# Optimization experiments

Hardware: AMD Instinct MI355X
Metric: run time of the kernel (lower is better)

Reference implementation:

```python
import jax, jax.numpy as jnp
import numpy as np

G = 8  # order of C8 rotation group

def expand_circulant(w):
    # w: [out_fields, in_fields, G] free params of a C8 regular->regular 1x1 conv.
    # Full weight: W[of*G+go, if*G+gi] = w[of, if, (go-gi) mod G]
    g = jnp.arange(G)
    idx = (g[:, None] - g[None, :]) % G            # [go, gi]
    Wf = w[:, :, idx]                              # [of, if, go, gi]
    Wf = jnp.transpose(Wf, (0, 2, 1, 3))           # [of, go, if, gi]
    return Wf.reshape(w.shape[0] * G, w.shape[1] * G)

def eq_proj(x2, w, b):
    # x2: [B, in_fields*G]; equivariant 1x1 conv = GEMM with circulant-expanded weight
    Wf = expand_circulant(w)                       # [out_fields*G, in_fields*G]
    bf = jnp.repeat(b, G)                          # per-field bias, shared across group dim
    return x2 @ Wf.T + bf

def setup_inputs() -> dict:
    key = jax.random.key(0)
    ks = jax.random.split(key, 12)
    B, d_model, n_head, d_k, d_v = 8192, 128, 8, 64, 64
    C = d_model * G                                # 1024
    s_in = 0.02
    inp = {
        'q': jax.random.normal(ks[0], (B, C, 1, 1), jnp.float32),
        'k': jax.random.normal(ks[1], (B, C, 1, 1), jnp.float32),
        'v': jax.random.normal(ks[2], (B, C, 1, 1), jnp.float32),
        'w_q': jax.random.normal(ks[3], (n_head * d_k, d_model, G), jnp.float32) * s_in,
        'b_q': jnp.zeros((n_head * d_k,), jnp.float32),
        'w_k': jax.random.normal(ks[4], (n_head * d_k, d_model, G), jnp.float32) * s_in,
        'b_k': jnp.zeros((n_head * d_k,), jnp.float32),
        'w_v': jax.random.normal(ks[5], (n_head * d_v, d_model, G), jnp.float32) * s_in,
        'b_v': jnp.zeros((n_head * d_v,), jnp.float32),
        'w_fc': jax.random.normal(ks[6], (d_model, n_head * d_v, G), jnp.float32) * s_in,
        'b_fc': jnp.zeros((d_model,), jnp.float32),
    }
    return inp

def reference(q, k, v, w_q, b_q, w_k, b_k, w_v, b_v, w_fc, b_fc):
    B, C = q.shape[0], q.shape[1]
    n_head, d_k = 8, 64
    d_v = 64
    temp = jnp.asarray(d_k ** 0.5, q.dtype)
    residual = q                                   # [B, C, 1, 1]
    q2 = q.reshape(B, C)
    k2 = k.reshape(B, C)
    v2 = v.reshape(B, C)
    # equivariant 1x1 conv projections -> [B, n_head*d_k*G]
    qp = eq_proj(q2, w_q, b_q).reshape(B, G, n_head, d_k).transpose(0, 2, 1, 3)  # [B,H,G,dk]
    kp = eq_proj(k2, w_k, b_k).reshape(B, G, n_head, d_k).transpose(0, 2, 1, 3)
    vp = eq_proj(v2, w_v, b_v).reshape(B, G, n_head, d_v).transpose(0, 2, 1, 3)
    # scaled dot-product attention over the G=8 group/orientation positions
    attn = jax.nn.softmax(jnp.einsum('bhqd,bhkd->bhqk', qp / temp, kp), axis=-1)  # [B,H,G,G]
    out = jnp.einsum('bhqk,bhkd->bhqd', attn, vp)  # [B,H,G,dv]
    # transpose(1,2) then flatten, exactly as torch .view(sz_b, -1, 1, 1)
    out = out.transpose(0, 2, 1, 3).reshape(B, G * n_head * d_v)
    out = eq_proj(out, w_fc, b_fc)                 # [B, d_model*G]
    out = out.reshape(B, C, 1, 1) + residual
    return out, attn
```

## Files before the change

### kernel.cpp

```cpp
#include <hip/hip_runtime.h>
#include <hip/hip_bf16.h>

typedef unsigned short u16;
typedef unsigned int u32;
typedef __bf16 bf16x8_t __attribute__((ext_vector_type(8)));
typedef float f32x4_t __attribute__((ext_vector_type(4)));

#define BK 64

__device__ __forceinline__ float b2f(u16 v) {
  return __uint_as_float(((u32)v) << 16);
}
__device__ __forceinline__ u16 f2b(float f) {
  __hip_bfloat16 h = __float2bfloat16(f);
  return *reinterpret_cast<u16*>(&h);
}
__device__ __forceinline__ float blo(u32 u) { return __uint_as_float(u << 16); }
__device__ __forceinline__ float bhi(u32 u) { return __uint_as_float(u & 0xffff0000u); }

__device__ __forceinline__ void async_lds16(const u16* g, u16* l) {
  __builtin_amdgcn_global_load_lds(
      (__attribute__((address_space(1))) void*)g,
      (__attribute__((address_space(3))) void*)l, 16, 0, 0);
}

__device__ __forceinline__ void expand8(const float* __restrict__ w,
                                        u16* __restrict__ dst, int I,
                                        int kshift, int gid) {
  const int n = gid >> kshift;
  const int kc = (gid & ((1 << kshift) - 1)) * 8;
  const int K = 8 << kshift;
  const float* wp = w + (size_t)((n >> 3) * I + (kc >> 3)) * 8;
  float4 w0 = *(const float4*)wp;
  float4 w1 = *(const float4*)(wp + 4);
  float w8[8] = {w0.x, w0.y, w0.z, w0.w, w1.x, w1.y, w1.z, w1.w};
  u16 t[8];
  const int r = (n - kc) & 7;
#pragma unroll
  for (int j = 0; j < 8; ++j) t[j] = f2b(w8[(r - j) & 7]);
  *(uint4*)(dst + (size_t)n * K + kc) = *(const uint4*)t;
}

__device__ __forceinline__ void cvt8(const float* __restrict__ src,
                                     u16* __restrict__ dst, int gid) {
  const float* p = src + (size_t)gid * 8;
  float4 a = *(const float4*)p;
  float4 b = *(const float4*)(p + 4);
  u16 t[8] = {f2b(a.x), f2b(a.y), f2b(a.z), f2b(a.w),
              f2b(b.x), f2b(b.y), f2b(b.z), f2b(b.w)};
  *(uint4*)(dst + (size_t)gid * 8) = *(const uint4*)t;
}

__global__ __launch_bounds__(256) void expand_all(
    const float* __restrict__ w_q, const float* __restrict__ w_k,
    const float* __restrict__ w_v, const float* __restrict__ w_fc,
    const float* __restrict__ q, const float* __restrict__ k,
    const float* __restrict__ v, u16* __restrict__ Wq, u16* __restrict__ Wk,
    u16* __restrict__ Wv, u16* __restrict__ Wfc, u16* __restrict__ qb,
    u16* __restrict__ kb, u16* __restrict__ vb, int cblocks) {
  const int e = blockIdx.x;
  if (e < 8192) {
    const int plane = e >> 11;
    const int gid = (e & 2047) * 256 + threadIdx.x;
    if (plane == 0) expand8(w_q, Wq, 128, 7, gid);
    else if (plane == 1) expand8(w_k, Wk, 128, 7, gid);
    else if (plane == 2) expand8(w_v, Wv, 128, 7, gid);
    else expand8(w_fc, Wfc, 512, 9, gid);
  } else {
    const int ce = e - 8192;
    const int plane = ce / cblocks;
    const int gid = (ce - plane * cblocks) * 256 + threadIdx.x;
    if (plane == 0) cvt8(q, qb, gid);
    else if (plane == 1) cvt8(k, kb, gid);
    else cvt8(v, vb, gid);
  }
}

template <int TN, bool HAS_RES, bool OUT_F32>
__device__ __forceinline__ void gemm_core(
    const u16* __restrict__ Xb, const u16* __restrict__ W,
    const float* __restrict__ bias, const float* __restrict__ res,
    void* __restrict__ Yv, int M, int N, int K, int bid) {
  __shared__ __align__(16) u16 As[128 * BK];
  __shared__ __align__(16) u16 Bs[TN * BK];
  const int tid = threadIdx.x;

  const int grid_m = M >> 7, grid_n = N / TN;
  const int nb = grid_m * grid_n;
  int pid = (bid & 7) * (nb >> 3) + (bid >> 3);
  const int nig = 8 * grid_n;
  const int group_id = pid / nig;
  const int first_m = group_id * 8;
  const int gsz = min(8, grid_m - first_m);
  const int mt = first_m + (pid % gsz);
  const int nt = (pid % nig) / gsz;
  const int m0 = mt << 7, n0 = nt * TN;

  const int lane = tid & 63;
  const int wave = tid >> 6;
  const int wm = (wave >> 1) * 64;
  const int wn = (wave & 1) * (TN / 2);
  const int l16 = lane & 15;
  const int quad = lane >> 4;
  constexpr int NJ = TN >> 5;

  f32x4_t acc[4][NJ] = {};

  const int row0 = tid >> 3;
  const int kgl = ((tid & 7) ^ (row0 & 7)) * 8;

  for (int k0 = 0; k0 < K; k0 += BK) {
#pragma unroll
    for (int it = 0; it < TN / 32; ++it)
      async_lds16(W + (size_t)(n0 + row0 + it * 32) * K + (k0 + kgl),
                  &Bs[(tid + it * 256) * 8]);
#pragma unroll
    for (int it = 0; it < 4; ++it)
      async_lds16(Xb + (size_t)(m0 + row0 + it * 32) * K + (k0 + kgl),
                  &As[(tid + it * 256) * 8]);
    __syncthreads();
#pragma unroll
    for (int half = 0; half < 2; ++half) {
      bf16x8_t af[4], bfr[NJ];
#pragma unroll
      for (int i = 0; i < 4; ++i)
        af[i] = *(const bf16x8_t*)&As[(wm + i * 16 + l16) * BK +
                                      (((quad + half * 4) ^ (l16 & 7)) * 8)];
#pragma unroll
      for (int j = 0; j < NJ; ++j)
        bfr[j] = *(const bf16x8_t*)&Bs[(wn + j * 16 + l16) * BK +
                                       (((quad + half * 4) ^ (l16 & 7)) * 8)];
#pragma unroll
      for (int i = 0; i < 4; ++i)
#pragma unroll
        for (int j = 0; j < NJ; ++j)
          acc[i][j] =
              __builtin_amdgcn_mfma_f32_16x16x32_bf16(af[i], bfr[j], acc[i][j], 0, 0, 0);
    }
    __syncthreads();
  }

#pragma unroll
  for (int j = 0; j < NJ; ++j) {
    const int col = n0 + wn + j * 16 + l16;
    const float bv = bias[col >> 3];
#pragma unroll
    for (int i = 0; i < 4; ++i) {
#pragma unroll
      for (int r = 0; r < 4; ++r) {
        const int rw = m0 + wm + i * 16 + quad * 4 + r;
        float vv = acc[i][j][r] + bv;
        if (HAS_RES) vv += res[(size_t)rw * N + col];
        if (OUT_F32)
          ((float*)Yv)[(size_t)rw * N + col] = vv;
        else
          ((u16*)Yv)[(size_t)rw * N + col] = f2b(vv);
      }
    }
  }
}

__global__ __launch_bounds__(256) void gemm_qkv(
    const u16* __restrict__ X0, const u16* __restrict__ X1,
    const u16* __restrict__ X2, const u16* __restrict__ W0,
    const u16* __restrict__ W1, const u16* __restrict__ W2,
    const float* __restrict__ b0, const float* __restrict__ b1,
    const float* __restrict__ b2, u16* __restrict__ Y0, u16* __restrict__ Y1,
    u16* __restrict__ Y2, int M, int N, int K) {
  const int z = blockIdx.y;
  const u16* X = (z == 0) ? X0 : (z == 1) ? X1 : X2;
  const u16* W = (z == 0) ? W0 : (z == 1) ? W1 : W2;
  const float* bb = (z == 0) ? b0 : (z == 1) ? b1 : b2;
  u16* Y = (z == 0) ? Y0 : (z == 1) ? Y1 : Y2;
  gemm_core<128, false, false>(X, W, bb, nullptr, Y, M, N, K, blockIdx.x);
}

__global__ __launch_bounds__(256) void gemm_fc(
    const u16* __restrict__ X, const u16* __restrict__ W,
    const float* __restrict__ bias, const float* __restrict__ res,
    float* __restrict__ Y, int M, int N, int K) {
  gemm_core<128, true, true>(X, W, bias, res, Y, M, N, K, blockIdx.x);
}

__global__ __launch_bounds__(256) void attn_kernel(
    const u16* __restrict__ qp, const u16* __restrict__ kp,
    const u16* __restrict__ vp, float* __restrict__ probs,
    u16* __restrict__ o, int iters) {
  __shared__ __align__(16) u16 Qs[4][8 * 72];
  __shared__ __align__(16) u16 Ks[4][8 * 72];
  __shared__ __align__(16) float Ps[4][64];
  const int tid = threadIdx.x;
  const int wave = tid >> 6;
  const int lane = tid & 63;
  const int r = lane >> 3, c = lane & 7;
  const int ls = r * 72 + c * 8;
  const int qg = r;
  const int kg = c;

  auto pairof = [&](int it) { return (it * gridDim.x + blockIdx.x) * 4 + wave; };
  auto gaddr = [&](int it) {
    const int pr = pairof(it);
    return (size_t)(pr >> 3) * 4096 + (size_t)r * 512 + (pr & 7) * 64 + c * 8;
  };

  uint4 qr = *(const uint4*)(qp + gaddr(0));
  uint4 kr = *(const uint4*)(kp + gaddr(0));

  for (int it = 0; it < iters; ++it) {
    *(uint4*)&Qs[wave][ls] = qr;
    *(uint4*)&Ks[wave][ls] = kr;
    const int pair = pairof(it);
    const int b = pair >> 3;
    const int h = pair & 7;
    float vcf[8];
#pragma unroll
    for (int k2 = 0; k2 < 8; ++k2)
      vcf[k2] = b2f(vp[(size_t)b * 4096 + (size_t)k2 * 512 + h * 64 + lane]);
    if (it + 1 < iters) {
      qr = *(const uint4*)(qp + gaddr(it + 1));
      kr = *(const uint4*)(kp + gaddr(it + 1));
    }
    float s = 0.f;
#pragma unroll
    for (int d8 = 0; d8 < 8; ++d8) {
      uint4 qa = *(const uint4*)&Qs[wave][qg * 72 + d8 * 8];
      uint4 ka = *(const uint4*)&Ks[wave][kg * 72 + d8 * 8];
      s += blo(qa.x) * blo(ka.x) + bhi(qa.x) * bhi(ka.x);
      s += blo(qa.y) * blo(ka.y) + bhi(qa.y) * bhi(ka.y);
      s += blo(qa.z) * blo(ka.z) + bhi(qa.z) * bhi(ka.z);
      s += blo(qa.w) * blo(ka.w) + bhi(qa.w) * bhi(ka.w);
    }
    s *= 0.125f;
    float mx = s;
    mx = fmaxf(mx, __shfl_xor(mx, 1));
    mx = fmaxf(mx, __shfl_xor(mx, 2));
    mx = fmaxf(mx, __shfl_xor(mx, 4));
    float e = __expf(s - mx);
    float sum = e;
    sum += __shfl_xor(sum, 1);
    sum += __shfl_xor(sum, 2);
    sum += __shfl_xor(sum, 4);
    const float p = e / sum;
    probs[(size_t)pair * 64 + lane] = p;
    Ps[wave][lane] = p;
#pragma unroll
    for (int q2 = 0; q2 < 8; ++q2) {
      float4 p0 = *(const float4*)&Ps[wave][q2 * 8];
      float4 p1 = *(const float4*)&Ps[wave][q2 * 8 + 4];
      float acc = p0.x * vcf[0] + p0.y * vcf[1] + p0.z * vcf[2] + p0.w * vcf[3] +
                  p1.x * vcf[4] + p1.y * vcf[5] + p1.z * vcf[6] + p1.w * vcf[7];
      o[(size_t)b * 4096 + q2 * 512 + h * 64 + lane] = f2b(acc);
    }
  }
}

extern "C" void kernel_launch(void* const* d_in, const int* in_sizes, int n_in,
                              void* d_out, int out_size, void* d_ws, size_t ws_size,
                              hipStream_t stream) {
  const float* q = (const float*)d_in[0];
  const float* k = (const float*)d_in[1];
  const float* v = (const float*)d_in[2];
  const float* w_q = (const float*)d_in[3];
  const float* b_q = (const float*)d_in[4];
  const float* w_k = (const float*)d_in[5];
  const float* b_k = (const float*)d_in[6];
  const float* w_v = (const float*)d_in[7];
  const float* b_v = (const float*)d_in[8];
  const float* w_fc = (const float*)d_in[9];
  const float* b_fc = (const float*)d_in[10];

  const int B = in_sizes[0] / 1024;
  float* out = (float*)d_out;
  float* probs = out + (size_t)B * 1024;

  u16* Wq = (u16*)d_ws;
  u16* Wk = Wq + (size_t)4096 * 1024;
  u16* Wv = Wk + (size_t)4096 * 1024;
  u16* Wfc = Wv + (size_t)4096 * 1024;
  u16* qb = Wfc + (size_t)4096 * 1024;
  u16* kb = qb + (size_t)B * 1024;
  u16* vb = kb + (size_t)B * 1024;
  u16* scratch = vb + (size_t)B * 1024;
  const size_t fixed_bytes =
      ((size_t)4 * 4096 * 1024 + (size_t)3 * B * 1024) * sizeof(u16);

  const size_t per_row = (size_t)(4 * 4096) * sizeof(u16);
  int chunkB = 128;
  for (int c = B; c >= 128; c >>= 1) {
    if (fixed_bytes + (size_t)c * per_row <= ws_size) { chunkB = c; break; }
  }

  u16* qp = scratch;
  u16* kp = qp + (size_t)chunkB * 4096;
  u16* vp = kp + (size_t)chunkB * 4096;
  u16* ao = vp + (size_t)chunkB * 4096;

  const int cblocks = B / 2;
  expand_all<<<8192 + 3 * cblocks, 256, 0, stream>>>(
      w_q, w_k, w_v, w_fc, q, k, v, Wq, Wk, Wv, Wfc, qb, kb, vb, cblocks);

  for (int cs = 0; cs < B; cs += chunkB) {
    const int nb_p = (chunkB / 128) * (4096 / 128);
    gemm_qkv<<<dim3(nb_p, 3), 256, 0, stream>>>(
        qb + (size_t)cs * 1024, kb + (size_t)cs * 1024, vb + (size_t)cs * 1024,
        Wq, Wk, Wv, b_q, b_k, b_v, qp, kp, vp, chunkB, 4096, 1024);
    const int ablocks = (chunkB >= 1024) ? 2048 : chunkB * 2;
    const int aiters = (chunkB * 8) / (ablocks * 4);
    attn_kernel<<<ablocks, 256, 0, stream>>>(qp, kp, vp,
                                             probs + (size_t)cs * 512, ao, aiters);
    const int nb_fc = (chunkB / 128) * (1024 / 128);
    gemm_fc<<<nb_fc, 256, 0, stream>>>(ao, Wfc, b_fc, q + (size_t)cs * 1024,
                                       out + (size_t)cs * 1024, chunkB, 1024,
                                       4096);
  }
}
```

Baseline: 677.4 us.

## Add 256x256-tile 4-stage pipelined QKV GEMM and narrow FC GEMM tile

Replaces the QKV projection GEMM with a dedicated 512-thread kernel that uses 256x256 output tiles, BK=32, and a 4-deep asynchronous global-to-LDS pipeline with explicit vmcnt waits and MFMA priority boosting. Each wave now computes 128x64, which raises arithmetic intensity and hides memory latency behind more stages. The FC GEMM switches to 64-wide N tiles so it launches more blocks, and the minimum chunk size goes up to 256 to match the new tiling. The larger tile costs more registers and 128KB of LDS per block, which may limit occupancy.

```diff
diff --git a/kernel.cpp b/kernel.cpp
--- a/kernel.cpp
+++ b/kernel.cpp
@@ -76,6 +76,111 @@
   }
 }
 
+__global__ __launch_bounds__(512, 2) void gemm_qkv256(
+    const u16* __restrict__ X0, const u16* __restrict__ X1,
+    const u16* __restrict__ X2, const u16* __restrict__ W0,
+    const u16* __restrict__ W1, const u16* __restrict__ W2,
+    const float* __restrict__ b0, const float* __restrict__ b1,
+    const float* __restrict__ b2, u16* __restrict__ Y0, u16* __restrict__ Y1,
+    u16* __restrict__ Y2, int M, int N, int K) {
+  __shared__ __align__(16) u16 lds[4 * 16384];
+  const int z = blockIdx.y;
+  const u16* X = (z == 0) ? X0 : (z == 1) ? X1 : X2;
+  const u16* W = (z == 0) ? W0 : (z == 1) ? W1 : W2;
+  const float* bias = (z == 0) ? b0 : (z == 1) ? b1 : b2;
+  u16* Y = (z == 0) ? Y0 : (z == 1) ? Y1 : Y2;
+
+  const int tid = threadIdx.x;
+  const int bid = blockIdx.x;
+  const int grid_m = M >> 8, grid_n = N >> 8;
+  const int nb = grid_m * grid_n;
+  int pid = (bid & 7) * (nb >> 3) + (bid >> 3);
+  const int nig = 8 * grid_n;
+  const int group_id = pid / nig;
+  const int first_m = group_id * 8;
+  const int gsz = min(8, grid_m - first_m);
+  const int mt = first_m + (pid % gsz);
+  const int ntile = (pid % nig) / gsz;
+  const int m0 = mt << 8, n0 = ntile << 8;
+
+  const int lane = tid & 63, wave = tid >> 6;
+  const int wm = (wave >> 2) * 128;
+  const int wn = (wave & 3) * 64;
+  const int l16 = lane & 15, quad = lane >> 4;
+  const int kbl = quad ^ ((l16 >> 1) & 3);
+
+  const int srow = tid >> 2;
+  const int skbg = (tid & 3) ^ ((tid >> 3) & 3);
+  const u16* pA = X + (size_t)(m0 + srow) * K + skbg * 8;
+  const u16* pB = W + (size_t)(n0 + srow) * K + skbg * 8;
+  const size_t rskip = (size_t)128 * K;
+
+  const int aoff = (wm + l16) * 32 + kbl * 8;
+  const int boff = 8192 + (wn + l16) * 32 + kbl * 8;
+
+  f32x4_t acc[8][4] = {};
+  const int nt = K >> 5;
+
+  auto stage = [&](int t) {
+    u16* l = lds + (t & 3) * 16384;
+    const u16* a = pA + t * 32;
+    const u16* b = pB + t * 32;
+    async_lds16(a, l + tid * 8);
+    async_lds16(a + rskip, l + tid * 8 + 4096);
+    async_lds16(b, l + 8192 + tid * 8);
+    async_lds16(b + rskip, l + 8192 + tid * 8 + 4096);
+  };
+
+  stage(0);
+  __builtin_amdgcn_sched_barrier(0);
+  stage(1);
+  __builtin_amdgcn_sched_barrier(0);
+  stage(2);
+  asm volatile("s_waitcnt vmcnt(8)" ::: "memory");
+  __builtin_amdgcn_s_barrier();
+  __builtin_amdgcn_sched_barrier(0);
+
+  for (int t = 0; t < nt; ++t) {
+    if (t + 3 < nt) stage(t + 3);
+    const u16* la = lds + (t & 3) * 16384 + aoff;
+    const u16* lb = lds + (t & 3) * 16384 + boff;
+    bf16x8_t a[8], b[4];
+#pragma unroll
+    for (int mi = 0; mi < 8; ++mi) a[mi] = *(const bf16x8_t*)(la + mi * 512);
+#pragma unroll
+    for (int ni = 0; ni < 4; ++ni) b[ni] = *(const bf16x8_t*)(lb + ni * 512);
+    __builtin_amdgcn_s_setprio(1);
+#pragma unroll
+    for (int mi = 0; mi < 8; ++mi)
+#pragma unroll
+      for (int ni = 0; ni < 4; ++ni)
+        acc[mi][ni] = __builtin_amdgcn_mfma_f32_16x16x32_bf16(a[mi], b[ni],
+                                                              acc[mi][ni], 0, 0, 0);
+    __builtin_amdgcn_s_setprio(0);
+    if (t + 1 < nt) {
+      if (t + 3 < nt)      asm volatile("s_waitcnt vmcnt(8)" ::: "memory");
+      else if (t + 2 < nt) asm volatile("s_waitcnt vmcnt(4)" ::: "memory");
+      else                 asm volatile("s_waitcnt vmcnt(0)" ::: "memory");
+      __builtin_amdgcn_s_barrier();
+      __builtin_amdgcn_sched_barrier(0);
+    }
+  }
+
+#pragma unroll
+  for (int ni = 0; ni < 4; ++ni) {
+    const int col = n0 + wn + ni * 16 + l16;
+    const float bv = bias[col >> 3];
+#pragma unroll
+    for (int mi = 0; mi < 8; ++mi) {
+#pragma unroll
+      for (int r = 0; r < 4; ++r) {
+        const int rw = m0 + wm + mi * 16 + quad * 4 + r;
+        Y[(size_t)rw * N + col] = f2b(acc[mi][ni][r] + bv);
+      }
+    }
+  }
+}
+
 template <int TN, bool HAS_RES, bool OUT_F32>
 __device__ __forceinline__ void gemm_core(
     const u16* __restrict__ Xb, const u16* __restrict__ W,
@@ -160,26 +265,11 @@
   }
 }
 
-__global__ __launch_bounds__(256) void gemm_qkv(
-    const u16* __restrict__ X0, const u16* __restrict__ X1,
-    const u16* __restrict__ X2, const u16* __restrict__ W0,
-    const u16* __restrict__ W1, const u16* __restrict__ W2,
-    const float* __restrict__ b0, const float* __restrict__ b1,
-    const float* __restrict__ b2, u16* __restrict__ Y0, u16* __restrict__ Y1,
-    u16* __restrict__ Y2, int M, int N, int K) {
-  const int z = blockIdx.y;
-  const u16* X = (z == 0) ? X0 : (z == 1) ? X1 : X2;
-  const u16* W = (z == 0) ? W0 : (z == 1) ? W1 : W2;
-  const float* bb = (z == 0) ? b0 : (z == 1) ? b1 : b2;
-  u16* Y = (z == 0) ? Y0 : (z == 1) ? Y1 : Y2;
-  gemm_core<128, false, false>(X, W, bb, nullptr, Y, M, N, K, blockIdx.x);
-}
-
 __global__ __launch_bounds__(256) void gemm_fc(
     const u16* __restrict__ X, const u16* __restrict__ W,
     const float* __restrict__ bias, const float* __restrict__ res,
     float* __restrict__ Y, int M, int N, int K) {
-  gemm_core<128, true, true>(X, W, bias, res, Y, M, N, K, blockIdx.x);
+  gemm_core<64, true, true>(X, W, bias, res, Y, M, N, K, blockIdx.x);
 }
 
 __global__ __launch_bounds__(256) void attn_kernel(
@@ -285,8 +375,8 @@
       ((size_t)4 * 4096 * 1024 + (size_t)3 * B * 1024) * sizeof(u16);
 
   const size_t per_row = (size_t)(4 * 4096) * sizeof(u16);
-  int chunkB = 128;
-  for (int c = B; c >= 128; c >>= 1) {
+  int chunkB = 256;
+  for (int c = B; c >= 256; c >>= 1) {
     if (fixed_bytes + (size_t)c * per_row <= ws_size) { chunkB = c; break; }
   }
 
@@ -300,15 +390,15 @@
       w_q, w_k, w_v, w_fc, q, k, v, Wq, Wk, Wv, Wfc, qb, kb, vb, cblocks);
 
   for (int cs = 0; cs < B; cs += chunkB) {
-    const int nb_p = (chunkB / 128) * (4096 / 128);
-    gemm_qkv<<<dim3(nb_p, 3), 256, 0, stream>>>(
+    const int nb_p = (chunkB / 256) * (4096 / 256);
+    gemm_qkv256<<<dim3(nb_p, 3), 512, 0, stream>>>(
         qb + (size_t)cs * 1024, kb + (size_t)cs * 1024, vb + (size_t)cs * 1024,
         Wq, Wk, Wv, b_q, b_k, b_v, qp, kp, vp, chunkB, 4096, 1024);
     const int ablocks = (chunkB >= 1024) ? 2048 : chunkB * 2;
     const int aiters = (chunkB * 8) / (ablocks * 4);
     attn_kernel<<<ablocks, 256, 0, stream>>>(qp, kp, vp,
                                              probs + (size_t)cs * 512, ao, aiters);
-    const int nb_fc = (chunkB / 128) * (1024 / 128);
+    const int nb_fc = (chunkB / 128) * (1024 / 64);
     gemm_fc<<<nb_fc, 256, 0, stream>>>(ao, Wfc, b_fc, q + (size_t)cs * 1024,
                                        out + (size_t)cs * 1024, chunkB, 1024,
                                        4096);
```

Result: faster. 612.1 us (-9.6%).
